# Optimization experiments

Hardware: AMD Instinct MI355X
Metric: run time of the kernel (lower is better)

Reference implementation:

```python
import jax, jax.numpy as jnp
import numpy as np

B, T, S, H, NUM_HEAD = 4, 1024, 1024, 1024, 16
CAUSAL = True
EPS = 1e-5            # torch nn.LayerNorm default
NEG = -float(2 ** 32)  # masked_fill value in the source


def setup_inputs() -> dict:
    key = jax.random.key(0)
    ks = jax.random.split(key, 8)
    queries = jax.random.normal(ks[0], (B, T, H), jnp.float32)
    keys = jax.random.normal(ks[1], (B, S, H), jnp.float32)
    queries_mask = jax.random.randint(ks[2], (B, T, 1), 0, 2).astype(jnp.int32)
    keys_mask = jax.random.randint(ks[3], (B, S, 1), 0, 2).astype(jnp.int32)
    Wq = jax.random.normal(ks[4], (H, H), jnp.float32) * 0.02
    Wk = jax.random.normal(ks[5], (H, H), jnp.float32) * 0.02
    Wv = jax.random.normal(ks[6], (H, H), jnp.float32) * 0.02
    bq = jnp.zeros((H,), jnp.float32)
    bk = jnp.zeros((H,), jnp.float32)
    bv = jnp.zeros((H,), jnp.float32)
    gamma = jnp.ones((H,), jnp.float32)
    beta = jnp.zeros((H,), jnp.float32)
    return {"queries": queries, "queries_mask": queries_mask, "keys": keys,
            "keys_mask": keys_mask, "Wq": Wq, "bq": bq, "Wk": Wk, "bk": bk,
            "Wv": Wv, "bv": bv, "gamma": gamma, "beta": beta}


def _layernorm(x, gamma, beta):
    m = jnp.mean(x, axis=-1, keepdims=True)
    v = jnp.mean((x - m) ** 2, axis=-1, keepdims=True)  # biased var, as torch
    return gamma * (x - m) / jnp.sqrt(v + EPS) + beta


def reference(queries, queries_mask, keys, keys_mask, Wq, bq, Wk, bk, Wv, bv, gamma, beta):
    dh = H // NUM_HEAD
    # ReLU-activated QKV projections (torch Linear: x @ W.T + b)
    Q = jax.nn.relu(queries @ Wq.T + bq)            # (B,T,H)
    K = jax.nn.relu(keys @ Wk.T + bk)               # (B,S,H)
    V = jax.nn.relu(keys @ Wv.T + bv)               # (B,S,H)
    # chunk along feature dim then cat along batch == (h, B, L, dh) layout
    Qh = Q.reshape(B, T, NUM_HEAD, dh).transpose(2, 0, 1, 3)
    Kh = K.reshape(B, S, NUM_HEAD, dh).transpose(2, 0, 1, 3)
    Vh = V.reshape(B, S, NUM_HEAD, dh).transpose(2, 0, 1, 3)
    # scaled by sqrt(hidden_size), NOT sqrt(head_dim) — faithful to source
    scores = jnp.einsum('hbtd,hbsd->hbts', Qh, Kh) / float(np.sqrt(H))
    # padding mask via outer product of the two masks
    qm = queries_mask[..., 0].astype(jnp.float32)   # (B,T)
    km = keys_mask[..., 0].astype(jnp.float32)      # (B,S)
    pad = (qm[:, :, None] * km[:, None, :]) == 0.0  # (B,T,S) True -> masked
    scores = jnp.where(pad[None], NEG, scores)
    if CAUSAL:
        tri = jnp.triu(jnp.ones((T, S), bool), k=1)  # triu(ones)-eye == strict upper
        scores = jnp.where(tri[None, None], NEG, scores)
    attn = jax.nn.softmax(scores, axis=-1)
    out = jnp.einsum('hbts,hbsd->hbtd', attn, Vh)   # (h,B,T,dh)
    out = out.transpose(1, 2, 0, 3).reshape(B, T, H)  # cat heads back on feature dim
    out = out * queries_mask.astype(jnp.float32)
    return _layernorm(out + queries, gamma, beta)
```

## Files before the change

### kernel.cpp

```cpp
#include <hip/hip_runtime.h>
#include <hip/hip_bf16.h>
#include <math.h>

#define B_ 4
#define T_ 1024
#define S_ 1024
#define H_ 1024
#define NH_ 16
#define DH_ 64
#define NEGV -4294967296.0f
#define EPS_ 1e-5f

typedef __attribute__((ext_vector_type(8))) short short8;
typedef __attribute__((ext_vector_type(8))) unsigned short ushort8;
typedef __attribute__((ext_vector_type(4))) unsigned short ushort4v;
typedef __attribute__((ext_vector_type(4))) unsigned int uint4v;
typedef __attribute__((ext_vector_type(4))) float f32x4;

__device__ __forceinline__ unsigned short f2bf(float x) {
    unsigned int u = __float_as_uint(x);
    u += 0x7FFF + ((u >> 16) & 1);
    return (unsigned short)(u >> 16);
}

__device__ __forceinline__ float bf2f(unsigned short u) {
    return __uint_as_float(((unsigned int)u) << 16);
}

__device__ __forceinline__ unsigned int pack_bf16(float a, float b) {
    union { __hip_bfloat162 h; unsigned int u; } cv;
    cv.h = __float22bfloat162_rn(float2{a, b});
    return cv.u;
}

__device__ __forceinline__ void gload16(const unsigned short* g, unsigned short* l) {
    __builtin_amdgcn_global_load_lds(
        (const __attribute__((address_space(1))) unsigned int*)g,
        (__attribute__((address_space(3))) unsigned int*)l,
        16, 0, 0);
}

#define VMCNT(n) asm volatile("s_waitcnt vmcnt(" #n ")" ::: "memory")
#define LGKM0()  { asm volatile("s_waitcnt lgkmcnt(0)" ::: "memory"); \
                   __builtin_amdgcn_sched_barrier(0); }

__global__ __launch_bounds__(256) void cast_bf16(
    const float* __restrict__ q, const float* __restrict__ k,
    const float* __restrict__ wq, const float* __restrict__ wk,
    const float* __restrict__ wv,
    unsigned short* __restrict__ dq, unsigned short* __restrict__ dk,
    unsigned short* __restrict__ dwq, unsigned short* __restrict__ dwk,
    unsigned short* __restrict__ dwv)
{
    const int seg = blockIdx.y;
    const float* src; unsigned short* dst; int n;
    switch (seg) {
        case 0:  src = q;  dst = dq;  n = B_*T_*H_; break;
        case 1:  src = k;  dst = dk;  n = B_*S_*H_; break;
        case 2:  src = wq; dst = dwq; n = H_*H_;    break;
        case 3:  src = wk; dst = dwk; n = H_*H_;    break;
        default: src = wv; dst = dwv; n = H_*H_;    break;
    }
    const int i = (blockIdx.x * 256 + threadIdx.x) * 8;
    if (i >= n) return;
    float4 a = *(const float4*)&src[i];
    float4 b = *(const float4*)&src[i + 4];
    ushort8 o;
    o[0] = f2bf(a.x); o[1] = f2bf(a.y); o[2] = f2bf(a.z); o[3] = f2bf(a.w);
    o[4] = f2bf(b.x); o[5] = f2bf(b.y); o[6] = f2bf(b.z); o[7] = f2bf(b.w);
    *(ushort8*)&dst[i] = o;
}

template<int MH, int NH>
__device__ __forceinline__ void mfmaQ(f32x4 (&acc)[8][4],
                                      const short8 (&afr)[4][2],
                                      const short8 (&bfr)[2][2])
{
    #pragma unroll
    for (int i2 = 0; i2 < 4; ++i2)
        #pragma unroll
        for (int j2 = 0; j2 < 2; ++j2)
            #pragma unroll
            for (int kc = 0; kc < 2; ++kc)
                acc[MH*4+i2][NH*2+j2] = __builtin_amdgcn_mfma_f32_16x16x32_bf16(
                    afr[i2][kc], bfr[j2][kc], acc[MH*4+i2][NH*2+j2], 0, 0, 0);
}

__global__ __launch_bounds__(512) void qkv_mfma(
    const unsigned short* __restrict__ Xq, const unsigned short* __restrict__ Xk,
    const unsigned short* __restrict__ Wq, const unsigned short* __restrict__ Wk,
    const unsigned short* __restrict__ Wv,
    const float* __restrict__ bq, const float* __restrict__ bk,
    const float* __restrict__ bv,
    unsigned short* __restrict__ Qo, unsigned short* __restrict__ Ko,
    unsigned short* __restrict__ Vo)
{
    const int bi = (blockIdx.x & 7) * 24 + (blockIdx.x >> 3);
    const int col_t = bi >> 4, row_t = bi & 15;
    const int which = col_t >> 2;
    const int colW = (col_t & 3) * 256;
    const int row0 = row_t * 256;

    const unsigned short* X = (which == 0) ? Xq : Xk;
    const unsigned short* Wm = (which == 0) ? Wq : (which == 1) ? Wk : Wv;
    const float* bias        = (which == 0) ? bq : (which == 1) ? bk : bv;
    unsigned short* Out      = (which == 0) ? Qo : (which == 1) ? Ko : Vo;

    __shared__ __align__(16) unsigned short S[67584];

    const int tid = threadIdx.x;
    const int wid = tid >> 6, lane = tid & 63, lo = lane & 15, hi = lane >> 4;
    const int wm = wid >> 2, wn = wid & 3;
    const int swr = (lo & 7) << 3;
    const int csw = ((tid & 7) << 3) ^ (((tid >> 3) & 7) << 3);

    auto stageA = [&](int mh, int kt) {
        const int k0 = kt << 6;
        unsigned short* dst = &S[(kt & 1) * 32768 + mh * 8192 + wid * 512];
        #pragma unroll
        for (int u = 0; u < 2; ++u) {
            const int rowT = row0 + u * 128 + mh * 64 + (tid >> 3);
            gload16(&X[(size_t)rowT * H_ + k0 + csw], dst + u * 4096);
        }
    };
    auto stageB = [&](int nh, int kt) {
        const int k0 = kt << 6;
        unsigned short* dst = &S[(kt & 1) * 32768 + 16384 + nh * 8192 + wid * 512];
        #pragma unroll
        for (int u = 0; u < 2; ++u) {
            const int pr = u * 64 + (tid >> 3);
            const int n  = (pr >> 5) * 64 + nh * 32 + (pr & 31);
            gload16(&Wm[(size_t)(colW + n) * H_ + k0 + csw], dst + u * 4096);
        }
    };

    short8 afr[4][2], blo[2][2], bhi[2][2];
    f32x4 acc[8][4] = {};

    auto readA = [&](int boff, int mh) {
        #pragma unroll
        for (int i2 = 0; i2 < 4; ++i2)
            #pragma unroll
            for (int kc = 0; kc < 2; ++kc)
                afr[i2][kc] = *(const short8*)
                    &S[boff + mh*8192 + (wm*64 + i2*16 + lo)*64 + ((kc*32 + hi*8) ^ swr)];
    };
    auto readB = [&](int boff, int nh, short8 (&bf)[2][2]) {
        #pragma unroll
        for (int j2 = 0; j2 < 2; ++j2)
            #pragma unroll
            for (int kc = 0; kc < 2; ++kc)
                bf[j2][kc] = *(const short8*)
                    &S[boff + 16384 + nh*8192 + (wn*32 + j2*16 + lo)*64 + ((kc*32 + hi*8) ^ swr)];
    };

    stageA(0, 0); stageB(0, 0); stageA(1, 0); stageB(1, 0);
    stageA(0, 1); stageB(0, 1); stageA(1, 1); stageB(1, 1);
    VMCNT(0);
    __builtin_amdgcn_s_barrier();

    for (int it = 0; it < 16; ++it) {
        const int boff = (it & 1) * 32768;
        readA(boff, 0);
        readB(boff, 0, blo);
        if (it >= 1 && it <= 14) stageB(1, it + 1);
        __builtin_amdgcn_s_barrier();
        LGKM0();
        __builtin_amdgcn_s_setprio(1); mfmaQ<0,0>(acc, afr, blo); __builtin_amdgcn_s_setprio(0);
        __builtin_amdgcn_s_barrier();
        readB(boff, 1, bhi);
        if (it >= 1 && it <= 14) stageA(1, it + 1);
        __builtin_amdgcn_s_barrier();
        LGKM0();
        __builtin_amdgcn_s_setprio(1); mfmaQ<0,1>(acc, afr, bhi); __builtin_amdgcn_s_setprio(0);
        __builtin_amdgcn_s_barrier();
        readA(boff, 1);
        if (it <= 13) { stageA(0, it + 2); stageB(0, it + 2); }
        __builtin_amdgcn_s_barrier();
        LGKM0();
        __builtin_amdgcn_s_setprio(1);
        mfmaQ<1,0>(acc, afr, blo);
        mfmaQ<1,1>(acc, afr, bhi);
        __builtin_amdgcn_s_setprio(0);
        if (it < 14) { VMCNT(4); } else { VMCNT(0); }
        __builtin_amdgcn_s_barrier();
    }

    float bj[4];
    #pragma unroll
    for (int j = 0; j < 4; ++j)
        bj[j] = bias[colW + wn*64 + (j>>1)*32 + (j&1)*16 + lo];

    #pragma unroll
    for (int i = 0; i < 8; ++i) {
        const int er = wm*128 + (i>>2)*64 + (i&3)*16 + hi*4;
        #pragma unroll
        for (int j = 0; j < 4; ++j) {
            const int ec = wn*64 + (j>>1)*32 + (j&1)*16 + lo;
            #pragma unroll
            for (int r = 0; r < 4; ++r)
                S[(er + r) * 264 + ec] = f2bf(fmaxf(acc[i][j][r] + bj[j], 0.f));
        }
    }
    __syncthreads();
    #pragma unroll
    for (int u = 0; u < 16; ++u) {
        const int cid = u * 512 + tid;
        const int rr = cid >> 5, ch = cid & 31;
        ushort8 v = *(const ushort8*)&S[rr * 264 + ch * 8];
        *(ushort8*)&Out[(size_t)(row0 + rr) * H_ + colW + ch * 8] = v;
    }
}

__global__ __launch_bounds__(256) void vmean_prep(
    const unsigned short* __restrict__ V, const int* __restrict__ kmask,
    float* __restrict__ vmean_part, int* __restrict__ sfirst)
{
    const int bh = blockIdx.x >> 2, chunk = blockIdx.x & 3;
    const int b = bh >> 4, h = bh & 15;
    const int tid = threadIdx.x;
    const int d8 = tid & 7, sg = tid >> 3;

    __shared__ float red[32][68];
    __shared__ int sf_sh;
    if (tid == 0) sf_sh = S_;

    float acc[8] = {0,0,0,0,0,0,0,0};
    #pragma unroll
    for (int it = 0; it < 8; ++it) {
        const int s = chunk * 256 + sg + it * 32;
        ushort8 v = *(const ushort8*)&V[((size_t)b*S_ + s) * H_ + h*DH_ + d8*8];
        #pragma unroll
        for (int i = 0; i < 8; ++i) acc[i] += bf2f(v[i]);
    }
    #pragma unroll
    for (int i = 0; i < 8; ++i) red[sg][d8*8 + i] = acc[i];

    if (blockIdx.x < B_) {
        int lf = S_;
        #pragma unroll
        for (int u = 0; u < 4; ++u) {
            const int s = tid + u * 256;
            if (kmask[blockIdx.x * S_ + s] != 0) lf = min(lf, s);
        }
        atomicMin(&sf_sh, lf);
    }
    __syncthreads();

    for (int str = 16; str >= 1; str >>= 1) {
        if (sg < str) {
            #pragma unroll
            for (int i = 0; i < 8; ++i)
                red[sg][d8*8 + i] += red[sg + str][d8*8 + i];
        }
        __syncthreads();
    }
    if (tid < 64) vmean_part[blockIdx.x * 64 + tid] = red[0][tid] * (1.f / 1024.f);
    if (blockIdx.x < B_ && tid == 0) sfirst[blockIdx.x] = sf_sh;
}

__global__ __launch_bounds__(256) void attn_mfma(
    const unsigned short* __restrict__ Q, const unsigned short* __restrict__ K,
    const unsigned short* __restrict__ V, const int* __restrict__ kmask,
    const float* __restrict__ vmean_part, const int* __restrict__ sfirst,
    unsigned short* __restrict__ Ob)
{
    const int flat = blockIdx.x;
    const int nf = (flat & 7) * 64 + (flat >> 3);
    const int z = nf & 7, bh = nf >> 3;
    const int b = bh >> 4, h = bh & 15;

    const int tid = threadIdx.x;
    const int wid = tid >> 6, lane = tid & 63, hi = lane >> 4, lo = lane & 15;

    __shared__ unsigned short Ks[2][64][64];
    __shared__ unsigned short Vt[2][64][64];

    const int s_first = sfirst[b];

    const int srow = tid >> 2, d0k = (tid & 3) << 4, swk = (srow & 7) << 3;
    const int sp = tid & 31, dg = tid >> 5;
    const int s2 = sp * 2;
    const int ps = (s2 & 35) | ((s2 & 16) >> 2) | ((s2 & 12) << 1);

    ushort8 krA0, krA1, vrA0, vrA1; int kmA;
    ushort8 krB0, krB1, vrB0, vrB1; int kmB;

    auto stage_load = [&](int s0_, ushort8& k0, ushort8& k1,
                          ushort8& v0, ushort8& v1, int& kmr) {
        const unsigned short* kp = &K[((size_t)b*S_ + s0_ + srow) * H_ + h*DH_ + d0k];
        k0 = *(const ushort8*)kp;
        k1 = *(const ushort8*)(kp + 8);
        const unsigned short* vp = &V[((size_t)b*S_ + s0_ + s2) * H_ + h*DH_ + dg*8];
        v0 = *(const ushort8*)vp;
        v1 = *(const ushort8*)(vp + H_);
        kmr = kmask[b*S_ + s0_ + lane];
    };
    auto stage_write = [&](int pb, const ushort8& k0, const ushort8& k1,
                           const ushort8& v0, const ushort8& v1) {
        *(ushort8*)&Ks[pb][srow][d0k ^ swk]       = k0;
        *(ushort8*)&Ks[pb][srow][(d0k + 8) ^ swk] = k1;
        #pragma unroll
        for (int i = 0; i < 8; ++i) {
            const int d = dg*8 + i;
            const unsigned int pk = (unsigned int)(unsigned short)v0[i]
                                  | ((unsigned int)(unsigned short)v1[i] << 16);
            *(unsigned int*)&Vt[pb][d][ps ^ ((d & 7) << 3)] = pk;
        }
    };

    for (int item = 0; item < 2; ++item) {
        const int qt = item ? z : (15 - z);
        const int t0 = qt * 64;
        const int ntiles = qt + 1;
        const int tq = t0 + wid*16 + lo;

        short8 qf0, qf1;
        {
            const unsigned short* qp =
                &Q[((size_t)b*T_ + t0 + wid*16 + lo) * H_ + h*DH_ + hi*8];
            qf0 = *(const short8*)qp;
            qf1 = *(const short8*)(qp + 32);
        }

        float m = -INFINITY, l = 0.f;
        f32x4 oacc[4] = {{0,0,0,0},{0,0,0,0},{0,0,0,0},{0,0,0,0}};

        auto compute = [&](int pb, int s0, int kmr) {
            const unsigned long long kmb = __ballot(kmr != 0);
            f32x4 sc[4] = {{0,0,0,0},{0,0,0,0},{0,0,0,0},{0,0,0,0}};
            const int swq = (lo & 7) << 3;
            __builtin_amdgcn_s_setprio(1);
            #pragma unroll
            for (int n = 0; n < 4; ++n) {
                short8 kfa = *(const short8*)&Ks[pb][n*16 + lo][(hi*8) ^ swq];
                sc[n] = __builtin_amdgcn_mfma_f32_16x16x32_bf16(kfa, qf0, sc[n], 0, 0, 0);
                short8 kfb = *(const short8*)&Ks[pb][n*16 + lo][(32 + hi*8) ^ swq];
                sc[n] = __builtin_amdgcn_mfma_f32_16x16x32_bf16(kfb, qf1, sc[n], 0, 0, 0);
            }
            __builtin_amdgcn_s_setprio(0);
            float p[4][4];
            float rm = -INFINITY;
            #pragma unroll
            for (int n = 0; n < 4; ++n)
                #pragma unroll
                for (int r = 0; r < 4; ++r) {
                    const int sl = n*16 + hi*4 + r;
                    const bool msk = !((kmb >> sl) & 1ull) || (s0 + sl > tq);
                    const float v = sc[n][r] * 0.03125f;
                    p[n][r] = msk ? NEGV : v;
                    rm = fmaxf(rm, p[n][r]);
                }
            rm = fmaxf(rm, __shfl_xor(rm, 16));
            rm = fmaxf(rm, __shfl_xor(rm, 32));
            if (__any(rm > m + 8.f)) {
                const float mn  = fmaxf(m, rm);
                const float scl = __expf(m - mn);
                m = mn;
                l *= scl;
                #pragma unroll
                for (int r = 0; r < 4; ++r) {
                    const float os = __shfl(scl, hi*4 + r);
                    oacc[0][r] *= os; oacc[1][r] *= os;
                    oacc[2][r] *= os; oacc[3][r] *= os;
                }
            }
            float ts = 0.f;
            #pragma unroll
            for (int n = 0; n < 4; ++n)
                #pragma unroll
                for (int r = 0; r < 4; ++r) {
                    p[n][r] = __expf(p[n][r] - m);
                    ts += p[n][r];
                }
            ts += __shfl_xor(ts, 16);
            ts += __shfl_xor(ts, 32);
            l += ts;
            unsigned int pk0[4], pk1[4];
            #pragma unroll
            for (int n = 0; n < 4; ++n) {
                pk0[n] = pack_bf16(p[n][0], p[n][1]);
                pk1[n] = pack_bf16(p[n][2], p[n][3]);
            }
            __builtin_amdgcn_s_setprio(1);
            #pragma unroll
            for (int cch = 0; cch < 2; ++cch) {
                uint4v u;
                u.x = pk0[2*cch];   u.y = pk1[2*cch];
                u.z = pk0[2*cch+1]; u.w = pk1[2*cch+1];
                const short8 pf = __builtin_bit_cast(short8, u);
                #pragma unroll
                for (int n2 = 0; n2 < 4; ++n2) {
                    const int d = n2*16 + lo;
                    const short8 vf =
                        *(const short8*)&Vt[pb][d][(cch*32 + hi*8) ^ ((d & 7) << 3)];
                    oacc[n2] = __builtin_amdgcn_mfma_f32_16x16x32_bf16(pf, vf, oacc[n2], 0, 0, 0);
                }
            }
            __builtin_amdgcn_s_setprio(0);
        };

        __syncthreads();
        stage_load(0, krA0, krA1, vrA0, vrA1, kmA);
        int t = 0;
        for (;;) {
            stage_write(0, krA0, krA1, vrA0, vrA1);
            if (t + 1 < ntiles) stage_load((t+1) << 6, krB0, krB1, vrB0, vrB1, kmB);
            __syncthreads();
            compute(0, t << 6, kmA);
            if (++t >= ntiles) break;

            stage_write(1, krB0, krB1, vrB0, vrB1);
            if (t + 1 < ntiles) stage_load((t+1) << 6, krA0, krA1, vrA0, vrA1, kmA);
            __syncthreads();
            compute(1, t << 6, kmB);
            if (++t >= ntiles) break;
        }

        const float inv = 1.0f / l;
        #pragma unroll
        for (int r = 0; r < 4; ++r) {
            const float ir = __shfl(inv, hi*4 + r);
            const int trow = t0 + wid*16 + hi*4 + r;
            unsigned short* dst = &Ob[((size_t)b*T_ + trow) * H_ + h*DH_ + lo];
            if (trow < s_first) {
                #pragma unroll
                for (int g = 0; g < 4; ++g) {
                    float vm = vmean_part[(bh*4 + 0)*64 + lo + g*16]
                             + vmean_part[(bh*4 + 1)*64 + lo + g*16]
                             + vmean_part[(bh*4 + 2)*64 + lo + g*16]
                             + vmean_part[(bh*4 + 3)*64 + lo + g*16];
                    dst[g*16] = f2bf(vm);
                }
            } else {
                dst[0]  = f2bf(oacc[0][r] * ir);
                dst[16] = f2bf(oacc[1][r] * ir);
                dst[32] = f2bf(oacc[2][r] * ir);
                dst[48] = f2bf(oacc[3][r] * ir);
            }
        }
    }
}

__global__ __launch_bounds__(256) void ln_kernel(
    const unsigned short* __restrict__ Ob, float* __restrict__ Out,
    const float* __restrict__ queries, const int* __restrict__ qmask,
    const float* __restrict__ gamma, const float* __restrict__ beta)
{
    const int row = blockIdx.x;
    const int tid = threadIdx.x;
    const float qm = (float)qmask[row];

    ushort4v a4 = *(const ushort4v*)&Ob[(size_t)row * H_ + tid*4];
    float4 q4 = *(const float4*)&queries[(size_t)row * H_ + tid*4];
    float x0 = bf2f(a4.x) * qm + q4.x;
    float x1 = bf2f(a4.y) * qm + q4.y;
    float x2 = bf2f(a4.z) * qm + q4.z;
    float x3 = bf2f(a4.w) * qm + q4.w;

    float sum = x0 + x1 + x2 + x3;
    float sq  = x0*x0 + x1*x1 + x2*x2 + x3*x3;
    #pragma unroll
    for (int off = 32; off >= 1; off >>= 1) {
        sum += __shfl_down(sum, off);
        sq  += __shfl_down(sq,  off);
    }
    __shared__ float rs[4], rq[4];
    const int wid = tid >> 6, lane = tid & 63;
    if (lane == 0) { rs[wid] = sum; rq[wid] = sq; }
    __syncthreads();
    const float tot  = rs[0] + rs[1] + rs[2] + rs[3];
    const float totq = rq[0] + rq[1] + rq[2] + rq[3];
    const float mean = tot * (1.f / H_);
    const float var  = totq * (1.f / H_) - mean * mean;
    const float rstd = rsqrtf(var + EPS_);

    float4 g4 = *(const float4*)&gamma[tid*4];
    float4 b4 = *(const float4*)&beta[tid*4];
    float4 y;
    y.x = (x0 - mean) * rstd * g4.x + b4.x;
    y.y = (x1 - mean) * rstd * g4.y + b4.y;
    y.z = (x2 - mean) * rstd * g4.z + b4.z;
    y.w = (x3 - mean) * rstd * g4.w + b4.w;
    *(float4*)&Out[(size_t)row * H_ + tid*4] = y;
}

extern "C" void kernel_launch(void* const* d_in, const int* in_sizes, int n_in,
                              void* d_out, int out_size, void* d_ws, size_t ws_size,
                              hipStream_t stream)
{
    const float* queries = (const float*)d_in[0];
    const int*   qmask   = (const int*)  d_in[1];
    const float* keys    = (const float*)d_in[2];
    const int*   kmask   = (const int*)  d_in[3];
    const float* Wq      = (const float*)d_in[4];
    const float* bq      = (const float*)d_in[5];
    const float* Wk      = (const float*)d_in[6];
    const float* bk      = (const float*)d_in[7];
    const float* Wv      = (const float*)d_in[8];
    const float* bv      = (const float*)d_in[9];
    const float* gamma   = (const float*)d_in[10];
    const float* beta    = (const float*)d_in[11];
    float* out = (float*)d_out;

    unsigned short* Xqb = (unsigned short*)d_ws;
    unsigned short* Xkb = Xqb + (size_t)B_*T_*H_;
    unsigned short* Wqb = Xkb + (size_t)B_*S_*H_;
    unsigned short* Wkb = Wqb + (size_t)H_*H_;
    unsigned short* Wvb = Wkb + (size_t)H_*H_;
    unsigned short* Qb  = Wvb + (size_t)H_*H_;
    unsigned short* Kb  = Qb  + (size_t)B_*T_*H_;
    unsigned short* Vb  = Kb  + (size_t)B_*S_*H_;
    float* vmeanF = (float*)Xqb;
    int*   sfirstI = (int*)(vmeanF + 256*64);
    unsigned short* Ob = Xkb;

    dim3 gc((B_*T_*H_/8 + 255)/256, 5, 1);
    cast_bf16<<<gc, 256, 0, stream>>>(queries, keys, Wq, Wk, Wv,
                                      Xqb, Xkb, Wqb, Wkb, Wvb);

    qkv_mfma<<<192, 512, 0, stream>>>(Xqb, Xkb, Wqb, Wkb, Wvb,
                                      bq, bk, bv, Qb, Kb, Vb);

    vmean_prep<<<256, 256, 0, stream>>>(Vb, kmask, vmeanF, sfirstI);

    attn_mfma<<<512, 256, 0, stream>>>(Qb, Kb, Vb, kmask, vmeanF, sfirstI, Ob);

    ln_kernel<<<B_*T_, 256, 0, stream>>>(Ob, out, queries, qmask, gamma, beta);
}
```

Measured before the change: 95.40 us.

## Repipeline QKV GEMM loads and split attention into one query tile per block

The QKV GEMM main loop is unrolled by two k-steps with fixed LDS buffer offsets. Global-to-LDS staging is interleaved at finer granularity between the MFMA phases, with a partial VMCNT wait in the prologue and the bias load hoisted before the loop. The attention kernel drops the paired-work scheme (two query tiles per block, balanced long and short) and launches 1024 blocks of one query tile each, heaviest tiles first, with a launch-bounds occupancy hint. This aims to hide load latency in the GEMM and improve scheduling flexibility in attention, at the cost of more block overhead and a relaxed wait that depends on correct vmcnt accounting.

Measured after the change: 88.67 us. -7.1%, faster.

```diff
diff --git a/kernel.cpp b/kernel.cpp
--- a/kernel.cpp
+++ b/kernel.cpp
@@ -71,7 +71,7 @@
     *(ushort8*)&dst[i] = o;
 }
 
-template<int MH, int NH>
+template<int MH, int NHq>
 __device__ __forceinline__ void mfmaQ(f32x4 (&acc)[8][4],
                                       const short8 (&afr)[4][2],
                                       const short8 (&bfr)[2][2])
@@ -82,8 +82,8 @@
         for (int j2 = 0; j2 < 2; ++j2)
             #pragma unroll
             for (int kc = 0; kc < 2; ++kc)
-                acc[MH*4+i2][NH*2+j2] = __builtin_amdgcn_mfma_f32_16x16x32_bf16(
-                    afr[i2][kc], bfr[j2][kc], acc[MH*4+i2][NH*2+j2], 0, 0, 0);
+                acc[MH*4+i2][NHq*2+j2] = __builtin_amdgcn_mfma_f32_16x16x32_bf16(
+                    afr[i2][kc], bfr[j2][kc], acc[MH*4+i2][NHq*2+j2], 0, 0, 0);
 }
 
 __global__ __launch_bounds__(512) void qkv_mfma(
@@ -154,42 +154,68 @@
                     &S[boff + 16384 + nh*8192 + (wn*32 + j2*16 + lo)*64 + ((kc*32 + hi*8) ^ swr)];
     };
 
-    stageA(0, 0); stageB(0, 0); stageA(1, 0); stageB(1, 0);
-    stageA(0, 1); stageB(0, 1); stageA(1, 1); stageB(1, 1);
-    VMCNT(0);
+    float bj[4];
+    #pragma unroll
+    for (int j = 0; j < 4; ++j)
+        bj[j] = bias[colW + wn*64 + (j>>1)*32 + (j&1)*16 + lo];
+
+    stageA(0, 0); stageB(0, 0); stageB(1, 0); stageA(1, 0);
+    stageA(0, 1); stageB(0, 1); stageB(1, 1);
+    VMCNT(6);
     __builtin_amdgcn_s_barrier();
 
-    for (int it = 0; it < 16; ++it) {
-        const int boff = (it & 1) * 32768;
-        readA(boff, 0);
-        readB(boff, 0, blo);
-        if (it >= 1 && it <= 14) stageB(1, it + 1);
+    for (int i = 0; i < 8; ++i) {
+        const int kt = i * 2;
+        const bool st = (i <= 6);
+        readA(0, 0);
+        readB(0, 0, blo);
+        stageA(1, kt + 1);
         __builtin_amdgcn_s_barrier();
         LGKM0();
         __builtin_amdgcn_s_setprio(1); mfmaQ<0,0>(acc, afr, blo); __builtin_amdgcn_s_setprio(0);
         __builtin_amdgcn_s_barrier();
-        readB(boff, 1, bhi);
-        if (it >= 1 && it <= 14) stageA(1, it + 1);
+        readB(0, 1, bhi);
+        if (st) stageA(0, kt + 2);
         __builtin_amdgcn_s_barrier();
         LGKM0();
         __builtin_amdgcn_s_setprio(1); mfmaQ<0,1>(acc, afr, bhi); __builtin_amdgcn_s_setprio(0);
         __builtin_amdgcn_s_barrier();
-        readA(boff, 1);
-        if (it <= 13) { stageA(0, it + 2); stageB(0, it + 2); }
+        readA(0, 1);
+        if (st) stageB(0, kt + 2);
         __builtin_amdgcn_s_barrier();
         LGKM0();
-        __builtin_amdgcn_s_setprio(1);
-        mfmaQ<1,0>(acc, afr, blo);
-        mfmaQ<1,1>(acc, afr, bhi);
-        __builtin_amdgcn_s_setprio(0);
-        if (it < 14) { VMCNT(4); } else { VMCNT(0); }
-        __builtin_amdgcn_s_barrier();
-    }
-
-    float bj[4];
-    #pragma unroll
-    for (int j = 0; j < 4; ++j)
-        bj[j] = bias[colW + wn*64 + (j>>1)*32 + (j&1)*16 + lo];
+        __builtin_amdgcn_s_setprio(1); mfmaQ<1,0>(acc, afr, blo); __builtin_amdgcn_s_setprio(0);
+        __builtin_amdgcn_s_barrier();
+        if (st) stageB(1, kt + 2);
+        __builtin_amdgcn_s_barrier();
+        __builtin_amdgcn_s_setprio(1); mfmaQ<1,1>(acc, afr, bhi); __builtin_amdgcn_s_setprio(0);
+        if (st) { VMCNT(6); } else { VMCNT(0); }
+        __builtin_amdgcn_s_barrier();
+        readA(32768, 0);
+        readB(32768, 0, blo);
+        if (st) stageA(1, kt + 2);
+        __builtin_amdgcn_s_barrier();
+        LGKM0();
+        __builtin_amdgcn_s_setprio(1); mfmaQ<0,0>(acc, afr, blo); __builtin_amdgcn_s_setprio(0);
+        __builtin_amdgcn_s_barrier();
+        readB(32768, 1, bhi);
+        if (st) stageA(0, kt + 3);
+        __builtin_amdgcn_s_barrier();
+        LGKM0();
+        __builtin_amdgcn_s_setprio(1); mfmaQ<0,1>(acc, afr, bhi); __builtin_amdgcn_s_setprio(0);
+        __builtin_amdgcn_s_barrier();
+        readA(32768, 1);
+        if (st) stageB(0, kt + 3);
+        __builtin_amdgcn_s_barrier();
+        LGKM0();
+        __builtin_amdgcn_s_setprio(1); mfmaQ<1,0>(acc, afr, blo); __builtin_amdgcn_s_setprio(0);
+        __builtin_amdgcn_s_barrier();
+        if (st) stageB(1, kt + 3);
+        __builtin_amdgcn_s_barrier();
+        __builtin_amdgcn_s_setprio(1); mfmaQ<1,1>(acc, afr, bhi); __builtin_amdgcn_s_setprio(0);
+        if (st) { VMCNT(6); }
+        __builtin_amdgcn_s_barrier();
+    }
 
     #pragma unroll
     for (int i = 0; i < 8; ++i) {
@@ -259,15 +285,15 @@
     if (blockIdx.x < B_ && tid == 0) sfirst[blockIdx.x] = sf_sh;
 }
 
-__global__ __launch_bounds__(256) void attn_mfma(
+__global__ __launch_bounds__(256, 3) void attn_mfma(
     const unsigned short* __restrict__ Q, const unsigned short* __restrict__ K,
     const unsigned short* __restrict__ V, const int* __restrict__ kmask,
     const float* __restrict__ vmean_part, const int* __restrict__ sfirst,
     unsigned short* __restrict__ Ob)
 {
     const int flat = blockIdx.x;
-    const int nf = (flat & 7) * 64 + (flat >> 3);
-    const int z = nf & 7, bh = nf >> 3;
+    const int qt = 15 - (flat >> 6);
+    const int bh = (flat & 7) * 8 + ((flat >> 3) & 7);
     const int b = bh >> 4, h = bh & 15;
 
     const int tid = threadIdx.x;
@@ -309,135 +335,131 @@
         }
     };
 
-    for (int item = 0; item < 2; ++item) {
-        const int qt = item ? z : (15 - z);
-        const int t0 = qt * 64;
-        const int ntiles = qt + 1;
-        const int tq = t0 + wid*16 + lo;
-
-        short8 qf0, qf1;
-        {
-            const unsigned short* qp =
-                &Q[((size_t)b*T_ + t0 + wid*16 + lo) * H_ + h*DH_ + hi*8];
-            qf0 = *(const short8*)qp;
-            qf1 = *(const short8*)(qp + 32);
-        }
-
-        float m = -INFINITY, l = 0.f;
-        f32x4 oacc[4] = {{0,0,0,0},{0,0,0,0},{0,0,0,0},{0,0,0,0}};
-
-        auto compute = [&](int pb, int s0, int kmr) {
-            const unsigned long long kmb = __ballot(kmr != 0);
-            f32x4 sc[4] = {{0,0,0,0},{0,0,0,0},{0,0,0,0},{0,0,0,0}};
-            const int swq = (lo & 7) << 3;
-            __builtin_amdgcn_s_setprio(1);
-            #pragma unroll
-            for (int n = 0; n < 4; ++n) {
-                short8 kfa = *(const short8*)&Ks[pb][n*16 + lo][(hi*8) ^ swq];
-                sc[n] = __builtin_amdgcn_mfma_f32_16x16x32_bf16(kfa, qf0, sc[n], 0, 0, 0);
-                short8 kfb = *(const short8*)&Ks[pb][n*16 + lo][(32 + hi*8) ^ swq];
-                sc[n] = __builtin_amdgcn_mfma_f32_16x16x32_bf16(kfb, qf1, sc[n], 0, 0, 0);
+    const int t0 = qt * 64;
+    const int ntiles = qt + 1;
+    const int tq = t0 + wid*16 + lo;
+
+    short8 qf0, qf1;
+    {
+        const unsigned short* qp =
+            &Q[((size_t)b*T_ + t0 + wid*16 + lo) * H_ + h*DH_ + hi*8];
+        qf0 = *(const short8*)qp;
+        qf1 = *(const short8*)(qp + 32);
+    }
+
+    float m = -INFINITY, l = 0.f;
+    f32x4 oacc[4] = {{0,0,0,0},{0,0,0,0},{0,0,0,0},{0,0,0,0}};
+
+    auto compute = [&](int pb, int s0, int kmr) {
+        const unsigned long long kmb = __ballot(kmr != 0);
+        f32x4 sc[4] = {{0,0,0,0},{0,0,0,0},{0,0,0,0},{0,0,0,0}};
+        const int swq = (lo & 7) << 3;
+        __builtin_amdgcn_s_setprio(1);
+        #pragma unroll
+        for (int n = 0; n < 4; ++n) {
+            short8 kfa = *(const short8*)&Ks[pb][n*16 + lo][(hi*8) ^ swq];
+            sc[n] = __builtin_amdgcn_mfma_f32_16x16x32_bf16(kfa, qf0, sc[n], 0, 0, 0);
+            short8 kfb = *(const short8*)&Ks[pb][n*16 + lo][(32 + hi*8) ^ swq];
+            sc[n] = __builtin_amdgcn_mfma_f32_16x16x32_bf16(kfb, qf1, sc[n], 0, 0, 0);
+        }
+        __builtin_amdgcn_s_setprio(0);
+        float p[4][4];
+        float rm = -INFINITY;
+        #pragma unroll
+        for (int n = 0; n < 4; ++n)
+            #pragma unroll
+            for (int r = 0; r < 4; ++r) {
+                const int sl = n*16 + hi*4 + r;
+                const bool msk = !((kmb >> sl) & 1ull) || (s0 + sl > tq);
+                const float v = sc[n][r] * 0.03125f;
+                p[n][r] = msk ? NEGV : v;
+                rm = fmaxf(rm, p[n][r]);
             }
-            __builtin_amdgcn_s_setprio(0);
-            float p[4][4];
-            float rm = -INFINITY;
-            #pragma unroll
-            for (int n = 0; n < 4; ++n)
-                #pragma unroll
-                for (int r = 0; r < 4; ++r) {
-                    const int sl = n*16 + hi*4 + r;
-                    const bool msk = !((kmb >> sl) & 1ull) || (s0 + sl > tq);
-                    const float v = sc[n][r] * 0.03125f;
-                    p[n][r] = msk ? NEGV : v;
-                    rm = fmaxf(rm, p[n][r]);
-                }
-            rm = fmaxf(rm, __shfl_xor(rm, 16));
-            rm = fmaxf(rm, __shfl_xor(rm, 32));
-            if (__any(rm > m + 8.f)) {
-                const float mn  = fmaxf(m, rm);
-                const float scl = __expf(m - mn);
-                m = mn;
-                l *= scl;
-                #pragma unroll
-                for (int r = 0; r < 4; ++r) {
-                    const float os = __shfl(scl, hi*4 + r);
-                    oacc[0][r] *= os; oacc[1][r] *= os;
-                    oacc[2][r] *= os; oacc[3][r] *= os;
-                }
+        rm = fmaxf(rm, __shfl_xor(rm, 16));
+        rm = fmaxf(rm, __shfl_xor(rm, 32));
+        if (__any(rm > m + 8.f)) {
+            const float mn  = fmaxf(m, rm);
+            const float scl = __expf(m - mn);
+            m = mn;
+            l *= scl;
+            #pragma unroll
+            for (int r = 0; r < 4; ++r) {
+                const float os = __shfl(scl, hi*4 + r);
+                oacc[0][r] *= os; oacc[1][r] *= os;
+                oacc[2][r] *= os; oacc[3][r] *= os;
             }
-            float ts = 0.f;
-            #pragma unroll
-            for (int n = 0; n < 4; ++n)
-                #pragma unroll
-                for (int r = 0; r < 4; ++r) {
-                    p[n][r] = __expf(p[n][r] - m);
-                    ts += p[n][r];
-                }
-            ts += __shfl_xor(ts, 16);
-            ts += __shfl_xor(ts, 32);
-            l += ts;
-            unsigned int pk0[4], pk1[4];
-            #pragma unroll
-            for (int n = 0; n < 4; ++n) {
-                pk0[n] = pack_bf16(p[n][0], p[n][1]);
-                pk1[n] = pack_bf16(p[n][2], p[n][3]);
+        }
+        float ts = 0.f;
+        #pragma unroll
+        for (int n = 0; n < 4; ++n)
+            #pragma unroll
+            for (int r = 0; r < 4; ++r) {
+                p[n][r] = __expf(p[n][r] - m);
+                ts += p[n][r];
             }
-            __builtin_amdgcn_s_setprio(1);
-            #pragma unroll
-            for (int cch = 0; cch < 2; ++cch) {
-                uint4v u;
-                u.x = pk0[2*cch];   u.y = pk1[2*cch];
-                u.z = pk0[2*cch+1]; u.w = pk1[2*cch+1];
-                const short8 pf = __builtin_bit_cast(short8, u);
-                #pragma unroll
-                for (int n2 = 0; n2 < 4; ++n2) {
-                    const int d = n2*16 + lo;
-                    const short8 vf =
-                        *(const short8*)&Vt[pb][d][(cch*32 + hi*8) ^ ((d & 7) << 3)];
-                    oacc[n2] = __builtin_amdgcn_mfma_f32_16x16x32_bf16(pf, vf, oacc[n2], 0, 0, 0);
-                }
+        ts += __shfl_xor(ts, 16);
+        ts += __shfl_xor(ts, 32);
+        l += ts;
+        unsigned int pk0[4], pk1[4];
+        #pragma unroll
+        for (int n = 0; n < 4; ++n) {
+            pk0[n] = pack_bf16(p[n][0], p[n][1]);
+            pk1[n] = pack_bf16(p[n][2], p[n][3]);
+        }
+        __builtin_amdgcn_s_setprio(1);
+        #pragma unroll
+        for (int cch = 0; cch < 2; ++cch) {
+            uint4v u;
+            u.x = pk0[2*cch];   u.y = pk1[2*cch];
+            u.z = pk0[2*cch+1]; u.w = pk1[2*cch+1];
+            const short8 pf = __builtin_bit_cast(short8, u);
+            #pragma unroll
+            for (int n2 = 0; n2 < 4; ++n2) {
+                const int d = n2*16 + lo;
+                const short8 vf =
+                    *(const short8*)&Vt[pb][d][(cch*32 + hi*8) ^ ((d & 7) << 3)];
+                oacc[n2] = __builtin_amdgcn_mfma_f32_16x16x32_bf16(pf, vf, oacc[n2], 0, 0, 0);
             }
-            __builtin_amdgcn_s_setprio(0);
-        };
-
+        }
+        __builtin_amdgcn_s_setprio(0);
+    };
+
+    stage_load(0, krA0, krA1, vrA0, vrA1, kmA);
+    int t = 0;
+    for (;;) {
+        stage_write(0, krA0, krA1, vrA0, vrA1);
+        if (t + 1 < ntiles) stage_load((t+1) << 6, krB0, krB1, vrB0, vrB1, kmB);
         __syncthreads();
-        stage_load(0, krA0, krA1, vrA0, vrA1, kmA);
-        int t = 0;
-        for (;;) {
-            stage_write(0, krA0, krA1, vrA0, vrA1);
-            if (t + 1 < ntiles) stage_load((t+1) << 6, krB0, krB1, vrB0, vrB1, kmB);
-            __syncthreads();
-            compute(0, t << 6, kmA);
-            if (++t >= ntiles) break;
-
-            stage_write(1, krB0, krB1, vrB0, vrB1);
-            if (t + 1 < ntiles) stage_load((t+1) << 6, krA0, krA1, vrA0, vrA1, kmA);
-            __syncthreads();
-            compute(1, t << 6, kmB);
-            if (++t >= ntiles) break;
-        }
-
-        const float inv = 1.0f / l;
-        #pragma unroll
-        for (int r = 0; r < 4; ++r) {
-            const float ir = __shfl(inv, hi*4 + r);
-            const int trow = t0 + wid*16 + hi*4 + r;
-            unsigned short* dst = &Ob[((size_t)b*T_ + trow) * H_ + h*DH_ + lo];
-            if (trow < s_first) {
-                #pragma unroll
-                for (int g = 0; g < 4; ++g) {
-                    float vm = vmean_part[(bh*4 + 0)*64 + lo + g*16]
-                             + vmean_part[(bh*4 + 1)*64 + lo + g*16]
-                             + vmean_part[(bh*4 + 2)*64 + lo + g*16]
-                             + vmean_part[(bh*4 + 3)*64 + lo + g*16];
-                    dst[g*16] = f2bf(vm);
-                }
-            } else {
-                dst[0]  = f2bf(oacc[0][r] * ir);
-                dst[16] = f2bf(oacc[1][r] * ir);
-                dst[32] = f2bf(oacc[2][r] * ir);
-                dst[48] = f2bf(oacc[3][r] * ir);
+        compute(0, t << 6, kmA);
+        if (++t >= ntiles) break;
+
+        stage_write(1, krB0, krB1, vrB0, vrB1);
+        if (t + 1 < ntiles) stage_load((t+1) << 6, krA0, krA1, vrA0, vrA1, kmA);
+        __syncthreads();
+        compute(1, t << 6, kmB);
+        if (++t >= ntiles) break;
+    }
+
+    const float inv = 1.0f / l;
+    #pragma unroll
+    for (int r = 0; r < 4; ++r) {
+        const float ir = __shfl(inv, hi*4 + r);
+        const int trow = t0 + wid*16 + hi*4 + r;
+        unsigned short* dst = &Ob[((size_t)b*T_ + trow) * H_ + h*DH_ + lo];
+        if (trow < s_first) {
+            #pragma unroll
+            for (int g = 0; g < 4; ++g) {
+                float vm = vmean_part[(bh*4 + 0)*64 + lo + g*16]
+                         + vmean_part[(bh*4 + 1)*64 + lo + g*16]
+                         + vmean_part[(bh*4 + 2)*64 + lo + g*16]
+                         + vmean_part[(bh*4 + 3)*64 + lo + g*16];
+                dst[g*16] = f2bf(vm);
             }
+        } else {
+            dst[0]  = f2bf(oacc[0][r] * ir);
+            dst[16] = f2bf(oacc[1][r] * ir);
+            dst[32] = f2bf(oacc[2][r] * ir);
+            dst[48] = f2bf(oacc[3][r] * ir);
         }
     }
 }
@@ -524,7 +546,7 @@
 
     vmean_prep<<<256, 256, 0, stream>>>(Vb, kmask, vmeanF, sfirstI);
 
-    attn_mfma<<<512, 256, 0, stream>>>(Qb, Kb, Vb, kmask, vmeanF, sfirstI, Ob);
+    attn_mfma<<<1024, 256, 0, stream>>>(Qb, Kb, Vb, kmask, vmeanF, sfirstI, Ob);
 
     ln_kernel<<<B_*T_, 256, 0, stream>>>(Ob, out, queries, qmask, gamma, beta);
 }
```
